# Kernel tuning notes

Measured on AMD Instinct MI355X. Metric: run time of the kernel, lower is better.

Reference implementation:

```python
import jax, jax.numpy as jnp
import numpy as np

B, T, J, D = 64, 2048, 256, 200  # D = 2*hidden_size


def setup_inputs() -> dict:
    key = jax.random.key(0)
    k = jax.random.split(key, 6)
    scale = 1.0 / np.sqrt(D)
    return {
        "h": jax.random.normal(k[0], (B, T, D), dtype=jnp.float32),
        "u": jax.random.normal(k[1], (B, J, D), dtype=jnp.float32),
        "w_h": jax.random.normal(k[2], (D,), dtype=jnp.float32) * scale,
        "b_h": jnp.zeros((1,), dtype=jnp.float32),
        "w_u": jax.random.normal(k[3], (D,), dtype=jnp.float32) * scale,
        "b_u": jnp.zeros((1,), dtype=jnp.float32),
        "w_hu": jax.random.normal(k[4], (D,), dtype=jnp.float32) * scale,
        "b_hu": jnp.zeros((1,), dtype=jnp.float32),
    }


def reference(h, u, w_h, b_h, w_u, b_u, w_hu, b_hu):
    # Trilinear similarity s[b,t,j] = w_h.h_t + w_u.u_j + w_hu.(h_t*u_j) + bias
    # Decomposed: no (B,T,J,D) intermediate (same math as torch expand version).
    s = (jnp.einsum('btd,d->bt', h, w_h)[:, :, None]
         + jnp.einsum('bjd,d->bj', u, w_u)[:, None, :]
         + jnp.einsum('btd,bjd->btj', h * w_hu, u)
         + (b_h + b_u + b_hu))  # (B,T,J)
    a = jax.nn.softmax(s, axis=2)                      # context-to-query attention
    c2q = jnp.einsum('btj,bjd->btd', a, u)             # (B,T,D)
    b = jax.nn.softmax(jnp.max(s, axis=2), axis=1)     # (B,T) query-to-context
    q2c = jnp.einsum('bt,btd->bd', b, h)[:, None, :]   # (B,1,D), tiled over T
    g = jnp.concatenate(
        [h, c2q, h * c2q, h * jnp.broadcast_to(q2c, h.shape)], axis=-1)  # (B,T,4D)
    return g
```

## Files before the change

kernel.cpp:

```cpp
#include <hip/hip_runtime.h>
#include <math.h>


#define B_ 64
#define T_ 2048
#define J_ 256
#define D_ 200
#define DP 224
#define TM 64
#define JC 32
#define NCH (J_ / JC)
#define XS 232
#define TS 40
#define PS 40
#define CQS 228

typedef __attribute__((ext_vector_type(8))) short bf16x8;
typedef __attribute__((ext_vector_type(4))) float f32x4;

__device__ __forceinline__ ushort bf_hi(float v) {
  const unsigned uu = __float_as_uint(v);
  return (ushort)((uu + 0x7FFFu + ((uu >> 16) & 1u)) >> 16);
}
__device__ __forceinline__ float bf_f(ushort hh) {
  return __uint_as_float(((unsigned)hh) << 16);
}

__global__ __launch_bounds__(256) void k_cterm(
    const float* __restrict__ u, const float* __restrict__ w_u,
    const float* __restrict__ b_h, const float* __restrict__ b_u,
    const float* __restrict__ b_hu, float* __restrict__ cterm) {
  const int wave = (blockIdx.x * 256 + threadIdx.x) >> 6;
  const int lane = threadIdx.x & 63;
  if (wave >= B_ * J_) return;
  const float* row = u + (size_t)wave * D_;
  float p = 0.f;
  for (int d = lane; d < D_; d += 64) p += row[d] * w_u[d];
  for (int off = 32; off > 0; off >>= 1) p += __shfl_xor(p, off, 64);
  if (lane == 0) cterm[wave] = p + b_h[0] + b_u[0] + b_hu[0];
}

__global__ __launch_bounds__(256, 1) void k_main(
    const float* __restrict__ h, const float* __restrict__ u,
    const float* __restrict__ w_h, const float* __restrict__ w_hu,
    const float* __restrict__ cterm, float* __restrict__ g,
    float* __restrict__ m_out) {
  __shared__ __align__(16) ushort xbuf[2][TM][XS];
  __shared__ __align__(16) ushort ubuf[2][JC][XS];
  __shared__ __align__(16) ushort utb[2][DP][TS];
  __shared__ __align__(16) ushort pbuf[2][TM][PS];
  __shared__ float ctl[J_];
  __shared__ float rtl[TM];

  const int tid = threadIdx.x;
  const int b = blockIdx.y;
  const int t0 = blockIdx.x * TM;
  const int w = tid >> 6;
  const int l = tid & 63;
  const int c = l & 15;
  const int gq = l >> 4;
  const int w16 = w * 16;

  for (int i = tid; i < TM * 32; i += 256) {
    const int r = i >> 5, cc = 200 + (i & 31);
    xbuf[0][r][cc] = 0; xbuf[1][r][cc] = 0;
  }
  for (int i = tid; i < JC * 32; i += 256) {
    const int r = i >> 5, cc = 200 + (i & 31);
    ubuf[0][r][cc] = 0; ubuf[1][r][cc] = 0;
  }
  for (int i = tid; i < 24 * TS; i += 256) {
    const int r = 200 + i / TS, cc = i % TS;
    utb[0][r][cc] = 0; utb[1][r][cc] = 0;
  }
  for (int i = tid; i < TM * 50; i += 256) {
    const int r = i / 50, c4 = (i % 50) * 4;
    const float4 hv = *(const float4*)(h + ((size_t)(b * T_ + t0 + r)) * D_ + c4);
    const float4 wv = *(const float4*)(w_hu + c4);
    const float x0 = hv.x * wv.x, x1 = hv.y * wv.y, x2 = hv.z * wv.z, x3 = hv.w * wv.w;
    const ushort h0 = bf_hi(x0), h1 = bf_hi(x1), h2 = bf_hi(x2), h3 = bf_hi(x3);
    *(ushort4*)&xbuf[0][r][c4] = make_ushort4(h0, h1, h2, h3);
    *(ushort4*)&xbuf[1][r][c4] = make_ushort4(
        bf_hi(x0 - bf_f(h0)), bf_hi(x1 - bf_f(h1)),
        bf_hi(x2 - bf_f(h2)), bf_hi(x3 - bf_f(h3)));
  }
  ctl[tid] = cterm[b * J_ + tid];
  {
    const int r = tid >> 2, q = tid & 3;
    const float* hr = h + ((size_t)(b * T_ + t0 + r)) * D_;
    float p = 0.f;
    for (int d = q; d < D_; d += 4) p = fmaf(hr[d], w_h[d], p);
    p += __shfl_xor(p, 1, 4);
    p += __shfl_xor(p, 2, 4);
    if (q == 0) rtl[r] = p;
  }
  __syncthreads();

  float m_run[4] = {-INFINITY, -INFINITY, -INFINITY, -INFINITY};
  float l_run[4] = {0.f, 0.f, 0.f, 0.f};
  const f32x4 zz = {0.f, 0.f, 0.f, 0.f};
  f32x4 cacc[14];
#pragma unroll
  for (int dt = 0; dt < 14; ++dt) cacc[dt] = zz;

#pragma unroll 1
  for (int ch = 0; ch < NCH; ++ch) {
    const int j0 = ch * JC;
    const float* ub = u + ((size_t)(b * J_ + j0)) * D_;
    for (int i = tid; i < JC * 50; i += 256) {
      const int r = i / 50, c4 = (i % 50) * 4;
      const float4 uv = *(const float4*)(ub + (size_t)r * D_ + c4);
      const ushort h0 = bf_hi(uv.x), h1 = bf_hi(uv.y), h2 = bf_hi(uv.z), h3 = bf_hi(uv.w);
      const ushort q0 = bf_hi(uv.x - bf_f(h0)), q1 = bf_hi(uv.y - bf_f(h1)),
                   q2 = bf_hi(uv.z - bf_f(h2)), q3 = bf_hi(uv.w - bf_f(h3));
      *(ushort4*)&ubuf[0][r][c4] = make_ushort4(h0, h1, h2, h3);
      *(ushort4*)&ubuf[1][r][c4] = make_ushort4(q0, q1, q2, q3);
      utb[0][c4 + 0][r] = h0; utb[0][c4 + 1][r] = h1;
      utb[0][c4 + 2][r] = h2; utb[0][c4 + 3][r] = h3;
      utb[1][c4 + 0][r] = q0; utb[1][c4 + 1][r] = q1;
      utb[1][c4 + 2][r] = q2; utb[1][c4 + 3][r] = q3;
    }
    __syncthreads();

    f32x4 s_hh0 = zz, s_lh0 = zz, s_hl0 = zz, s_hh1 = zz, s_lh1 = zz, s_hl1 = zz;
#pragma unroll
    for (int ks = 0; ks < 7; ++ks) {
      const int k0 = ks * 32 + gq * 8;
      const bf16x8 ah  = *(const bf16x8*)&xbuf[0][w16 + c][k0];
      const bf16x8 al  = *(const bf16x8*)&xbuf[1][w16 + c][k0];
      const bf16x8 b0h = *(const bf16x8*)&ubuf[0][c][k0];
      const bf16x8 b0l = *(const bf16x8*)&ubuf[1][c][k0];
      const bf16x8 b1h = *(const bf16x8*)&ubuf[0][16 + c][k0];
      const bf16x8 b1l = *(const bf16x8*)&ubuf[1][16 + c][k0];
      s_hh0 = __builtin_amdgcn_mfma_f32_16x16x32_bf16(ah, b0h, s_hh0, 0, 0, 0);
      s_lh0 = __builtin_amdgcn_mfma_f32_16x16x32_bf16(al, b0h, s_lh0, 0, 0, 0);
      s_hl0 = __builtin_amdgcn_mfma_f32_16x16x32_bf16(ah, b0l, s_hl0, 0, 0, 0);
      s_hh1 = __builtin_amdgcn_mfma_f32_16x16x32_bf16(ah, b1h, s_hh1, 0, 0, 0);
      s_lh1 = __builtin_amdgcn_mfma_f32_16x16x32_bf16(al, b1h, s_lh1, 0, 0, 0);
      s_hl1 = __builtin_amdgcn_mfma_f32_16x16x32_bf16(ah, b1l, s_hl1, 0, 0, 0);
    }

    const float ct0 = ctl[j0 + c];
    const float ct1 = ctl[j0 + 16 + c];
    float a_r[4];
#pragma unroll
    for (int r = 0; r < 4; ++r) {
      const float rt_t = rtl[w16 + gq * 4 + r];
      const float s0 = ((s_hh0[r] + s_lh0[r]) + s_hl0[r]) + rt_t + ct0;
      const float s1 = ((s_hh1[r] + s_lh1[r]) + s_hl1[r]) + rt_t + ct1;
      float mx = fmaxf(s0, s1);
      mx = fmaxf(mx, __shfl_xor(mx, 8, 16));
      mx = fmaxf(mx, __shfl_xor(mx, 4, 16));
      mx = fmaxf(mx, __shfl_xor(mx, 2, 16));
      mx = fmaxf(mx, __shfl_xor(mx, 1, 16));
      const float mnew = fmaxf(m_run[r], mx);
      const float a = __expf(m_run[r] - mnew);
      const float p0 = __expf(s0 - mnew);
      const float p1 = __expf(s1 - mnew);
      float ps = p0 + p1;
      ps += __shfl_xor(ps, 8, 16);
      ps += __shfl_xor(ps, 4, 16);
      ps += __shfl_xor(ps, 2, 16);
      ps += __shfl_xor(ps, 1, 16);
      l_run[r] = l_run[r] * a + ps;
      m_run[r] = mnew;
      a_r[r] = a;
      const int pr = w16 + gq * 4 + r;
      const ushort p0h = bf_hi(p0), p1h = bf_hi(p1);
      pbuf[0][pr][c] = p0h;
      pbuf[0][pr][16 + c] = p1h;
      pbuf[1][pr][c] = bf_hi(p0 - bf_f(p0h));
      pbuf[1][pr][16 + c] = bf_hi(p1 - bf_f(p1h));
    }
    const f32x4 av = {a_r[0], a_r[1], a_r[2], a_r[3]};
#pragma unroll
    for (int dt = 0; dt < 14; ++dt) cacc[dt] *= av;

    const bf16x8 pah = *(const bf16x8*)&pbuf[0][w16 + c][gq * 8];
    const bf16x8 pal = *(const bf16x8*)&pbuf[1][w16 + c][gq * 8];
#pragma unroll
    for (int dt = 0; dt < 14; ++dt) {
      const bf16x8 bh = *(const bf16x8*)&utb[0][dt * 16 + c][gq * 8];
      const bf16x8 bl = *(const bf16x8*)&utb[1][dt * 16 + c][gq * 8];
      cacc[dt] = __builtin_amdgcn_mfma_f32_16x16x32_bf16(pah, bh, cacc[dt], 0, 0, 0);
      cacc[dt] = __builtin_amdgcn_mfma_f32_16x16x32_bf16(pal, bh, cacc[dt], 0, 0, 0);
      cacc[dt] = __builtin_amdgcn_mfma_f32_16x16x32_bf16(pah, bl, cacc[dt], 0, 0, 0);
    }
    __syncthreads();
  }

  if (c == 0) {
#pragma unroll
    for (int r = 0; r < 4; ++r) m_out[b * T_ + t0 + w16 + gq * 4 + r] = m_run[r];
  }
  const f32x4 invv = {1.f / l_run[0], 1.f / l_run[1], 1.f / l_run[2], 1.f / l_run[3]};
  float* cq = (float*)&xbuf[0][0][0];
#pragma unroll
  for (int dt = 0; dt < 14; ++dt) {
    const f32x4 cv = cacc[dt] * invv;
    const int d = dt * 16 + c;
    cq[(w16 + gq * 4 + 0) * CQS + d] = cv[0];
    cq[(w16 + gq * 4 + 1) * CQS + d] = cv[1];
    cq[(w16 + gq * 4 + 2) * CQS + d] = cv[2];
    cq[(w16 + gq * 4 + 3) * CQS + d] = cv[3];
  }
  __syncthreads();
  for (int i = tid; i < TM * 50; i += 256) {
    const int r = i / 50, c4 = (i % 50) * 4;
    const size_t row = (size_t)(b * T_ + t0 + r);
    const float4 hv = *(const float4*)(h + row * D_ + c4);
    const float4 cv = *(const float4*)(cq + r * CQS + c4);
    float* gb = g + row * (4 * D_);
    *(float4*)(gb + c4) = hv;
    *(float4*)(gb + D_ + c4) = cv;
    *(float4*)(gb + 2 * D_ + c4) =
        make_float4(hv.x * cv.x, hv.y * cv.y, hv.z * cv.z, hv.w * cv.w);
  }
}

__global__ __launch_bounds__(256) void k_stats(
    const float* __restrict__ m, float* __restrict__ Mb, float* __restrict__ iZb) {
  const int b = blockIdx.x, tid = threadIdx.x;
  __shared__ float redm[4], reds[4];
  const float* mb = m + b * T_;
  float mx = -INFINITY;
  for (int tt = tid; tt < T_; tt += 256) mx = fmaxf(mx, mb[tt]);
  for (int off = 32; off > 0; off >>= 1) mx = fmaxf(mx, __shfl_xor(mx, off, 64));
  if ((tid & 63) == 0) redm[tid >> 6] = mx;
  __syncthreads();
  const float M = fmaxf(fmaxf(redm[0], redm[1]), fmaxf(redm[2], redm[3]));
  float se = 0.f;
  for (int tt = tid; tt < T_; tt += 256) se += __expf(mb[tt] - M);
  for (int off = 32; off > 0; off >>= 1) se += __shfl_xor(se, off, 64);
  if ((tid & 63) == 0) reds[tid >> 6] = se;
  __syncthreads();
  if (tid == 0) {
    Mb[b] = M;
    iZb[b] = 1.f / (reds[0] + reds[1] + reds[2] + reds[3]);
  }
}

__global__ __launch_bounds__(256) void k_q2c(
    const float* __restrict__ h, const float* __restrict__ m,
    const float* __restrict__ Mb, const float* __restrict__ iZb,
    float* __restrict__ q2c) {
  const int b = blockIdx.y;
  const int t0 = blockIdx.x * 32;
  const int tid = threadIdx.x;
  __shared__ float wl[32];
  if (tid < 32) wl[tid] = __expf(m[b * T_ + t0 + tid] - Mb[b]) * iZb[b];
  __syncthreads();
  if (tid < D_) {
    float acc = 0.f;
    const float* hb = h + ((size_t)(b * T_ + t0)) * D_ + tid;
    for (int tt = 0; tt < 32; ++tt) acc = fmaf(wl[tt], hb[(size_t)tt * D_], acc);
    atomicAdd(&q2c[b * D_ + tid], acc);
  }
}

__global__ __launch_bounds__(256) void k_g3(
    const float* __restrict__ h, const float* __restrict__ q2c,
    float* __restrict__ g) {
  const unsigned i = blockIdx.x * 256u + threadIdx.x;
  if (i >= (unsigned)(B_ * T_ * D_)) return;
  const unsigned row = i / D_;
  const unsigned d = i - row * D_;
  const unsigned b = row >> 11;
  g[(size_t)row * (4 * D_) + 3 * D_ + d] = h[i] * q2c[b * D_ + d];
}

extern "C" void kernel_launch(void* const* d_in, const int* in_sizes, int n_in,
                              void* d_out, int out_size, void* d_ws, size_t ws_size,
                              hipStream_t stream) {
  const float* h    = (const float*)d_in[0];
  const float* u    = (const float*)d_in[1];
  const float* w_h  = (const float*)d_in[2];
  const float* b_h  = (const float*)d_in[3];
  const float* w_u  = (const float*)d_in[4];
  const float* b_u  = (const float*)d_in[5];
  const float* w_hu = (const float*)d_in[6];
  const float* b_hu = (const float*)d_in[7];
  float* g = (float*)d_out;

  float* ws    = (float*)d_ws;
  float* cterm = ws;
  float* m     = ws + 16384;
  float* Mb    = ws + 16384 + 131072;
  float* iZb   = Mb + 64;
  float* q2c   = iZb + 64;

  hipMemsetAsync(q2c, 0, (size_t)B_ * D_ * sizeof(float), stream);

  k_cterm<<<(B_ * J_) / 4, 256, 0, stream>>>(u, w_u, b_h, b_u, b_hu, cterm);
  k_main<<<dim3(T_ / TM, B_), 256, 0, stream>>>(h, u, w_h, w_hu, cterm, g, m);
  k_stats<<<B_, 256, 0, stream>>>(m, Mb, iZb);
  k_q2c<<<dim3(T_ / 32, B_), 256, 0, stream>>>(h, m, Mb, iZb, q2c);
  k_g3<<<(B_ * T_ * D_ + 255) / 256, 256, 0, stream>>>(h, q2c, g);
}
```

Before: 1.055 ms.

## Shrink shared memory for two blocks per CU, swizzle LDS, vectorize g3

Moves the h*w_hu A-operand from shared memory into registers. The u tiles, transposed-u and probability buffers now share a union with the c2q staging area, and the D padding drops from 224 to 208 (13 d-tiles), so shared memory shrinks enough for two blocks per CU (launch bounds raised to 2). The transposed u buffer is built with coalesced column reads and XOR-swizzled offsets, and the probability buffer is swizzled the same way, to reduce LDS bank conflicts. The final h*q2c kernel becomes a float4 grid-stride loop. Register pressure from the held A fragments could cause spills under the two-block limit.

Result: faster. 868.5 us (-17.7%).

```diff
diff --git a/kernel.cpp b/kernel.cpp
--- a/kernel.cpp
+++ b/kernel.cpp
@@ -6,14 +6,15 @@
 #define T_ 2048
 #define J_ 256
 #define D_ 200
-#define DP 224
 #define TM 64
 #define JC 32
 #define NCH (J_ / JC)
 #define XS 232
 #define TS 40
 #define PS 40
-#define CQS 228
+#define UTR 208
+#define NDT 13
+#define CQS 212
 
 typedef __attribute__((ext_vector_type(8))) short bf16x8;
 typedef __attribute__((ext_vector_type(4))) float f32x4;
@@ -40,17 +41,21 @@
   if (lane == 0) cterm[wave] = p + b_h[0] + b_u[0] + b_hu[0];
 }
 
-__global__ __launch_bounds__(256, 1) void k_main(
+__global__ __launch_bounds__(256, 2) void k_main(
     const float* __restrict__ h, const float* __restrict__ u,
     const float* __restrict__ w_h, const float* __restrict__ w_hu,
     const float* __restrict__ cterm, float* __restrict__ g,
     float* __restrict__ m_out) {
-  __shared__ __align__(16) ushort xbuf[2][TM][XS];
-  __shared__ __align__(16) ushort ubuf[2][JC][XS];
-  __shared__ __align__(16) ushort utb[2][DP][TS];
-  __shared__ __align__(16) ushort pbuf[2][TM][PS];
-  __shared__ float ctl[J_];
-  __shared__ float rtl[TM];
+  __shared__ __align__(16) union SMem {
+    struct {
+      ushort ubuf[2][JC][XS];
+      ushort utb[2][UTR][TS];
+      ushort pbuf[2][TM][PS];
+      float ctl[J_];
+      float rtl[TM];
+    } s;
+    float cq[TM][CQS];
+  } sm;
 
   const int tid = threadIdx.x;
   const int b = blockIdx.y;
@@ -61,30 +66,15 @@
   const int gq = l >> 4;
   const int w16 = w * 16;
 
-  for (int i = tid; i < TM * 32; i += 256) {
-    const int r = i >> 5, cc = 200 + (i & 31);
-    xbuf[0][r][cc] = 0; xbuf[1][r][cc] = 0;
-  }
   for (int i = tid; i < JC * 32; i += 256) {
     const int r = i >> 5, cc = 200 + (i & 31);
-    ubuf[0][r][cc] = 0; ubuf[1][r][cc] = 0;
-  }
-  for (int i = tid; i < 24 * TS; i += 256) {
+    sm.s.ubuf[0][r][cc] = 0; sm.s.ubuf[1][r][cc] = 0;
+  }
+  for (int i = tid; i < 8 * TS; i += 256) {
     const int r = 200 + i / TS, cc = i % TS;
-    utb[0][r][cc] = 0; utb[1][r][cc] = 0;
-  }
-  for (int i = tid; i < TM * 50; i += 256) {
-    const int r = i / 50, c4 = (i % 50) * 4;
-    const float4 hv = *(const float4*)(h + ((size_t)(b * T_ + t0 + r)) * D_ + c4);
-    const float4 wv = *(const float4*)(w_hu + c4);
-    const float x0 = hv.x * wv.x, x1 = hv.y * wv.y, x2 = hv.z * wv.z, x3 = hv.w * wv.w;
-    const ushort h0 = bf_hi(x0), h1 = bf_hi(x1), h2 = bf_hi(x2), h3 = bf_hi(x3);
-    *(ushort4*)&xbuf[0][r][c4] = make_ushort4(h0, h1, h2, h3);
-    *(ushort4*)&xbuf[1][r][c4] = make_ushort4(
-        bf_hi(x0 - bf_f(h0)), bf_hi(x1 - bf_f(h1)),
-        bf_hi(x2 - bf_f(h2)), bf_hi(x3 - bf_f(h3)));
-  }
-  ctl[tid] = cterm[b * J_ + tid];
+    sm.s.utb[0][r][cc] = 0; sm.s.utb[1][r][cc] = 0;
+  }
+  sm.s.ctl[tid] = cterm[b * J_ + tid];
   {
     const int r = tid >> 2, q = tid & 3;
     const float* hr = h + ((size_t)(b * T_ + t0 + r)) * D_;
@@ -92,33 +82,69 @@
     for (int d = q; d < D_; d += 4) p = fmaf(hr[d], w_h[d], p);
     p += __shfl_xor(p, 1, 4);
     p += __shfl_xor(p, 2, 4);
-    if (q == 0) rtl[r] = p;
+    if (q == 0) sm.s.rtl[r] = p;
+  }
+
+  bf16x8 xh[7], xl[7];
+  {
+    const float* hrow = h + ((size_t)(b * T_ + t0 + w16 + c)) * D_;
+#pragma unroll
+    for (int ks = 0; ks < 7; ++ks) {
+      const int k0 = ks * 32 + gq * 8;
+      bf16x8 vh = {0, 0, 0, 0, 0, 0, 0, 0};
+      bf16x8 vl = {0, 0, 0, 0, 0, 0, 0, 0};
+      if (k0 < 200) {
+        const float4 a = *(const float4*)(hrow + k0);
+        const float4 bq = *(const float4*)(hrow + k0 + 4);
+        const float4 wa = *(const float4*)(w_hu + k0);
+        const float4 wb = *(const float4*)(w_hu + k0 + 4);
+        float xe[8] = {a.x * wa.x, a.y * wa.y, a.z * wa.z, a.w * wa.w,
+                       bq.x * wb.x, bq.y * wb.y, bq.z * wb.z, bq.w * wb.w};
+#pragma unroll
+        for (int e = 0; e < 8; ++e) {
+          const ushort hh = bf_hi(xe[e]);
+          vh[e] = (short)hh;
+          vl[e] = (short)bf_hi(xe[e] - bf_f(hh));
+        }
+      }
+      xh[ks] = vh;
+      xl[ks] = vl;
+    }
   }
   __syncthreads();
 
   float m_run[4] = {-INFINITY, -INFINITY, -INFINITY, -INFINITY};
   float l_run[4] = {0.f, 0.f, 0.f, 0.f};
   const f32x4 zz = {0.f, 0.f, 0.f, 0.f};
-  f32x4 cacc[14];
-#pragma unroll
-  for (int dt = 0; dt < 14; ++dt) cacc[dt] = zz;
+  f32x4 cacc[NDT];
+#pragma unroll
+  for (int dt = 0; dt < NDT; ++dt) cacc[dt] = zz;
 
 #pragma unroll 1
   for (int ch = 0; ch < NCH; ++ch) {
     const int j0 = ch * JC;
     const float* ub = u + ((size_t)(b * J_ + j0)) * D_;
     for (int i = tid; i < JC * 50; i += 256) {
-      const int r = i / 50, c4 = (i % 50) * 4;
+      const int r = i / 50, c4 = (i - r * 50) * 4;
       const float4 uv = *(const float4*)(ub + (size_t)r * D_ + c4);
       const ushort h0 = bf_hi(uv.x), h1 = bf_hi(uv.y), h2 = bf_hi(uv.z), h3 = bf_hi(uv.w);
-      const ushort q0 = bf_hi(uv.x - bf_f(h0)), q1 = bf_hi(uv.y - bf_f(h1)),
-                   q2 = bf_hi(uv.z - bf_f(h2)), q3 = bf_hi(uv.w - bf_f(h3));
-      *(ushort4*)&ubuf[0][r][c4] = make_ushort4(h0, h1, h2, h3);
-      *(ushort4*)&ubuf[1][r][c4] = make_ushort4(q0, q1, q2, q3);
-      utb[0][c4 + 0][r] = h0; utb[0][c4 + 1][r] = h1;
-      utb[0][c4 + 2][r] = h2; utb[0][c4 + 3][r] = h3;
-      utb[1][c4 + 0][r] = q0; utb[1][c4 + 1][r] = q1;
-      utb[1][c4 + 2][r] = q2; utb[1][c4 + 3][r] = q3;
+      *(ushort4*)&sm.s.ubuf[0][r][c4] = make_ushort4(h0, h1, h2, h3);
+      *(ushort4*)&sm.s.ubuf[1][r][c4] = make_ushort4(
+          bf_hi(uv.x - bf_f(h0)), bf_hi(uv.y - bf_f(h1)),
+          bf_hi(uv.z - bf_f(h2)), bf_hi(uv.w - bf_f(h3)));
+    }
+    for (int i = tid; i < 8 * 200; i += 256) {
+      const int j4 = i / 200, d = i - j4 * 200;
+      const float v0 = ub[(size_t)(j4 * 4 + 0) * D_ + d];
+      const float v1 = ub[(size_t)(j4 * 4 + 1) * D_ + d];
+      const float v2 = ub[(size_t)(j4 * 4 + 2) * D_ + d];
+      const float v3 = ub[(size_t)(j4 * 4 + 3) * D_ + d];
+      const ushort h0 = bf_hi(v0), h1 = bf_hi(v1), h2 = bf_hi(v2), h3 = bf_hi(v3);
+      const int off = (((j4 >> 1) ^ ((d >> 3) & 3)) << 3) + ((j4 & 1) << 2);
+      *(ushort4*)&sm.s.utb[0][d][off] = make_ushort4(h0, h1, h2, h3);
+      *(ushort4*)&sm.s.utb[1][d][off] = make_ushort4(
+          bf_hi(v0 - bf_f(h0)), bf_hi(v1 - bf_f(h1)),
+          bf_hi(v2 - bf_f(h2)), bf_hi(v3 - bf_f(h3)));
     }
     __syncthreads();
 
@@ -126,26 +152,24 @@
 #pragma unroll
     for (int ks = 0; ks < 7; ++ks) {
       const int k0 = ks * 32 + gq * 8;
-      const bf16x8 ah  = *(const bf16x8*)&xbuf[0][w16 + c][k0];
-      const bf16x8 al  = *(const bf16x8*)&xbuf[1][w16 + c][k0];
-      const bf16x8 b0h = *(const bf16x8*)&ubuf[0][c][k0];
-      const bf16x8 b0l = *(const bf16x8*)&ubuf[1][c][k0];
-      const bf16x8 b1h = *(const bf16x8*)&ubuf[0][16 + c][k0];
-      const bf16x8 b1l = *(const bf16x8*)&ubuf[1][16 + c][k0];
-      s_hh0 = __builtin_amdgcn_mfma_f32_16x16x32_bf16(ah, b0h, s_hh0, 0, 0, 0);
-      s_lh0 = __builtin_amdgcn_mfma_f32_16x16x32_bf16(al, b0h, s_lh0, 0, 0, 0);
-      s_hl0 = __builtin_amdgcn_mfma_f32_16x16x32_bf16(ah, b0l, s_hl0, 0, 0, 0);
-      s_hh1 = __builtin_amdgcn_mfma_f32_16x16x32_bf16(ah, b1h, s_hh1, 0, 0, 0);
-      s_lh1 = __builtin_amdgcn_mfma_f32_16x16x32_bf16(al, b1h, s_lh1, 0, 0, 0);
-      s_hl1 = __builtin_amdgcn_mfma_f32_16x16x32_bf16(ah, b1l, s_hl1, 0, 0, 0);
-    }
-
-    const float ct0 = ctl[j0 + c];
-    const float ct1 = ctl[j0 + 16 + c];
+      const bf16x8 b0h = *(const bf16x8*)&sm.s.ubuf[0][c][k0];
+      const bf16x8 b0l = *(const bf16x8*)&sm.s.ubuf[1][c][k0];
+      const bf16x8 b1h = *(const bf16x8*)&sm.s.ubuf[0][16 + c][k0];
+      const bf16x8 b1l = *(const bf16x8*)&sm.s.ubuf[1][16 + c][k0];
+      s_hh0 = __builtin_amdgcn_mfma_f32_16x16x32_bf16(xh[ks], b0h, s_hh0, 0, 0, 0);
+      s_lh0 = __builtin_amdgcn_mfma_f32_16x16x32_bf16(xl[ks], b0h, s_lh0, 0, 0, 0);
+      s_hl0 = __builtin_amdgcn_mfma_f32_16x16x32_bf16(xh[ks], b0l, s_hl0, 0, 0, 0);
+      s_hh1 = __builtin_amdgcn_mfma_f32_16x16x32_bf16(xh[ks], b1h, s_hh1, 0, 0, 0);
+      s_lh1 = __builtin_amdgcn_mfma_f32_16x16x32_bf16(xl[ks], b1h, s_lh1, 0, 0, 0);
+      s_hl1 = __builtin_amdgcn_mfma_f32_16x16x32_bf16(xh[ks], b1l, s_hl1, 0, 0, 0);
+    }
+
+    const float ct0 = sm.s.ctl[j0 + c];
+    const float ct1 = sm.s.ctl[j0 + 16 + c];
     float a_r[4];
 #pragma unroll
     for (int r = 0; r < 4; ++r) {
-      const float rt_t = rtl[w16 + gq * 4 + r];
+      const float rt_t = sm.s.rtl[w16 + gq * 4 + r];
       const float s0 = ((s_hh0[r] + s_lh0[r]) + s_hl0[r]) + rt_t + ct0;
       const float s1 = ((s_hh1[r] + s_lh1[r]) + s_hl1[r]) + rt_t + ct1;
       float mx = fmaxf(s0, s1);
@@ -167,21 +191,26 @@
       a_r[r] = a;
       const int pr = w16 + gq * 4 + r;
       const ushort p0h = bf_hi(p0), p1h = bf_hi(p1);
-      pbuf[0][pr][c] = p0h;
-      pbuf[0][pr][16 + c] = p1h;
-      pbuf[1][pr][c] = bf_hi(p0 - bf_f(p0h));
-      pbuf[1][pr][16 + c] = bf_hi(p1 - bf_f(p1h));
+      const int o0 = (((c >> 3) ^ gq) << 3) + (c & 7);
+      const int o1 = ((((c >> 3) + 2) ^ gq) << 3) + (c & 7);
+      sm.s.pbuf[0][pr][o0] = p0h;
+      sm.s.pbuf[0][pr][o1] = p1h;
+      sm.s.pbuf[1][pr][o0] = bf_hi(p0 - bf_f(p0h));
+      sm.s.pbuf[1][pr][o1] = bf_hi(p1 - bf_f(p1h));
     }
     const f32x4 av = {a_r[0], a_r[1], a_r[2], a_r[3]};
 #pragma unroll
-    for (int dt = 0; dt < 14; ++dt) cacc[dt] *= av;
-
-    const bf16x8 pah = *(const bf16x8*)&pbuf[0][w16 + c][gq * 8];
-    const bf16x8 pal = *(const bf16x8*)&pbuf[1][w16 + c][gq * 8];
-#pragma unroll
-    for (int dt = 0; dt < 14; ++dt) {
-      const bf16x8 bh = *(const bf16x8*)&utb[0][dt * 16 + c][gq * 8];
-      const bf16x8 bl = *(const bf16x8*)&utb[1][dt * 16 + c][gq * 8];
+    for (int dt = 0; dt < NDT; ++dt) cacc[dt] *= av;
+
+    const int psw = (gq ^ ((c >> 2) & 3)) << 3;
+    const bf16x8 pah = *(const bf16x8*)&sm.s.pbuf[0][w16 + c][psw];
+    const bf16x8 pal = *(const bf16x8*)&sm.s.pbuf[1][w16 + c][psw];
+#pragma unroll
+    for (int dt = 0; dt < NDT; ++dt) {
+      const int du = dt * 16 + c;
+      const int osw = (gq ^ ((du >> 3) & 3)) << 3;
+      const bf16x8 bh = *(const bf16x8*)&sm.s.utb[0][du][osw];
+      const bf16x8 bl = *(const bf16x8*)&sm.s.utb[1][du][osw];
       cacc[dt] = __builtin_amdgcn_mfma_f32_16x16x32_bf16(pah, bh, cacc[dt], 0, 0, 0);
       cacc[dt] = __builtin_amdgcn_mfma_f32_16x16x32_bf16(pal, bh, cacc[dt], 0, 0, 0);
       cacc[dt] = __builtin_amdgcn_mfma_f32_16x16x32_bf16(pah, bl, cacc[dt], 0, 0, 0);
@@ -194,22 +223,21 @@
     for (int r = 0; r < 4; ++r) m_out[b * T_ + t0 + w16 + gq * 4 + r] = m_run[r];
   }
   const f32x4 invv = {1.f / l_run[0], 1.f / l_run[1], 1.f / l_run[2], 1.f / l_run[3]};
-  float* cq = (float*)&xbuf[0][0][0];
-#pragma unroll
-  for (int dt = 0; dt < 14; ++dt) {
+#pragma unroll
+  for (int dt = 0; dt < NDT; ++dt) {
     const f32x4 cv = cacc[dt] * invv;
     const int d = dt * 16 + c;
-    cq[(w16 + gq * 4 + 0) * CQS + d] = cv[0];
-    cq[(w16 + gq * 4 + 1) * CQS + d] = cv[1];
-    cq[(w16 + gq * 4 + 2) * CQS + d] = cv[2];
-    cq[(w16 + gq * 4 + 3) * CQS + d] = cv[3];
+    sm.cq[w16 + gq * 4 + 0][d] = cv[0];
+    sm.cq[w16 + gq * 4 + 1][d] = cv[1];
+    sm.cq[w16 + gq * 4 + 2][d] = cv[2];
+    sm.cq[w16 + gq * 4 + 3][d] = cv[3];
   }
   __syncthreads();
   for (int i = tid; i < TM * 50; i += 256) {
-    const int r = i / 50, c4 = (i % 50) * 4;
+    const int r = i / 50, c4 = (i - r * 50) * 4;
     const size_t row = (size_t)(b * T_ + t0 + r);
     const float4 hv = *(const float4*)(h + row * D_ + c4);
-    const float4 cv = *(const float4*)(cq + r * CQS + c4);
+    const float4 cv = *(const float4*)(&sm.cq[r][c4]);
     float* gb = g + row * (4 * D_);
     *(float4*)(gb + c4) = hv;
     *(float4*)(gb + D_ + c4) = cv;
@@ -261,12 +289,16 @@
 __global__ __launch_bounds__(256) void k_g3(
     const float* __restrict__ h, const float* __restrict__ q2c,
     float* __restrict__ g) {
-  const unsigned i = blockIdx.x * 256u + threadIdx.x;
-  if (i >= (unsigned)(B_ * T_ * D_)) return;
-  const unsigned row = i / D_;
-  const unsigned d = i - row * D_;
-  const unsigned b = row >> 11;
-  g[(size_t)row * (4 * D_) + 3 * D_ + d] = h[i] * q2c[b * D_ + d];
+  const int n4 = B_ * T_ * D_ / 4;
+  for (int i = blockIdx.x * 256 + threadIdx.x; i < n4; i += gridDim.x * 256) {
+    const int row = i / 50;
+    const int d4 = i - row * 50;
+    const int b = row >> 11;
+    const float4 hv = *(const float4*)(h + (size_t)i * 4);
+    const float4 qv = *(const float4*)(q2c + b * D_ + d4 * 4);
+    *(float4*)(g + (size_t)row * (4 * D_) + 3 * D_ + d4 * 4) =
+        make_float4(hv.x * qv.x, hv.y * qv.y, hv.z * qv.z, hv.w * qv.w);
+  }
 }
 
 extern "C" void kernel_launch(void* const* d_in, const int* in_sizes, int n_in,
@@ -295,5 +327,5 @@
   k_main<<<dim3(T_ / TM, B_), 256, 0, stream>>>(h, u, w_h, w_hu, cterm, g, m);
   k_stats<<<B_, 256, 0, stream>>>(m, Mb, iZb);
   k_q2c<<<dim3(T_ / 32, B_), 256, 0, stream>>>(h, m, Mb, iZb, q2c);
-  k_g3<<<(B_ * T_ * D_ + 255) / 256, 256, 0, stream>>>(h, q2c, g);
-}
+  k_g3<<<4096, 256, 0, stream>>>(h, q2c, g);
+}
```
